# Kernel optimization log

Measured on AMD Instinct MI355X. Metric: run time of the kernel, lower is better.

Reference implementation:

```python
import jax, jax.numpy as jnp
import numpy as np

N = 50000
E = 640000
DIM_NODE = 128
DIM_HIDDEN = 128
DIM_FFN = 512
NUM_CLASSES = 10
NUM_GRAPHS = 128
NEG_SLOPE = 0.2


def setup_inputs() -> dict:
    key = jax.random.key(0)
    ks = jax.random.split(key, 24)
    g = lambda k, shape: jax.random.normal(k, shape, dtype=jnp.float32) * 0.05
    inp = {
        "x": jax.random.normal(ks[0], (N, DIM_NODE), dtype=jnp.float32),
        "edge_index": jax.random.randint(ks[1], (2, E), 0, N, dtype=jnp.int64),
        "batch": jnp.sort(jax.random.randint(ks[2], (N,), 0, NUM_GRAPHS, dtype=jnp.int64)),
        # GATConv 1: dim_node -> dim_hidden (heads=1)
        "W1": g(ks[3], (DIM_NODE, DIM_HIDDEN)),
        "as1": g(ks[4], (DIM_HIDDEN,)), "ad1": g(ks[5], (DIM_HIDDEN,)),
        "b1": g(ks[6], (DIM_HIDDEN,)),
        # GATConv 2
        "W2": g(ks[7], (DIM_HIDDEN, DIM_HIDDEN)),
        "as2": g(ks[8], (DIM_HIDDEN,)), "ad2": g(ks[9], (DIM_HIDDEN,)),
        "b2": g(ks[10], (DIM_HIDDEN,)),
        # GATConv 3
        "W3": g(ks[11], (DIM_HIDDEN, DIM_HIDDEN)),
        "as3": g(ks[12], (DIM_HIDDEN,)), "ad3": g(ks[13], (DIM_HIDDEN,)),
        "b3": g(ks[14], (DIM_HIDDEN,)),
        # FFN head
        "Wf1": g(ks[15], (DIM_HIDDEN, DIM_FFN)), "bf1": g(ks[16], (DIM_FFN,)),
        "Wf2": g(ks[17], (DIM_FFN, DIM_FFN)), "bf2": g(ks[18], (DIM_FFN,)),
        "Wf3": g(ks[19], (DIM_FFN, NUM_CLASSES)), "bf3": g(ks[20], (NUM_CLASSES,)),
    }
    return inp


def _gat_conv(x, src, dst, W, a_src, a_dst, bias):
    # x: [N, Fin]; src/dst: [E'] (self-loops included)
    h = x @ W                                  # [N, H]
    alpha_src = h @ a_src                      # [N]
    alpha_dst = h @ a_dst                      # [N]
    logits = jax.nn.leaky_relu(alpha_src[src] + alpha_dst[dst], NEG_SLOPE)  # [E']
    # segment softmax over incoming edges of each dst node
    m = jax.ops.segment_max(logits, dst, num_segments=N)
    ex = jnp.exp(logits - m[dst])
    denom = jax.ops.segment_sum(ex, dst, num_segments=N)
    alpha = ex / (denom[dst] + 1e-16)          # [E']
    out = jax.ops.segment_sum(alpha[:, None] * h[src], dst, num_segments=N)
    return out + bias


def reference(x, edge_index, batch, W1, as1, ad1, b1, W2, as2, ad2, b2,
              W3, as3, ad3, b3, Wf1, bf1, Wf2, bf2, Wf3, bf3):
    # PyG GATConv adds self-loops by default
    loops = jnp.arange(N, dtype=edge_index.dtype)
    src = jnp.concatenate([edge_index[0], loops])
    dst = jnp.concatenate([edge_index[1], loops])

    h = jax.nn.relu(_gat_conv(x, src, dst, W1, as1, ad1, b1))
    h = jax.nn.relu(_gat_conv(h, src, dst, W2, as2, ad2, b2))
    h = jax.nn.relu(_gat_conv(h, src, dst, W3, as3, ad3, b3))

    # global mean pool per graph
    sums = jax.ops.segment_sum(h, batch, num_segments=NUM_GRAPHS)
    cnts = jax.ops.segment_sum(jnp.ones((N,), h.dtype), batch, num_segments=NUM_GRAPHS)
    pooled = sums / jnp.maximum(cnts, 1.0)[:, None]   # [G, H]

    # FFN head (dropout is identity in eval)
    z = jax.nn.relu(pooled @ Wf1 + bf1)
    z = jax.nn.relu(z @ Wf2 + bf2)
    return z @ Wf3 + bf3                               # [G, num_classes]
```

## Files before the change

### kernel.cpp

```cpp
#include <hip/hip_runtime.h>

#define N_NODES 50000
#define N_EDGES 640000
#define TOT_E (N_EDGES + N_NODES)
#define NB 196
#define BCAP 4608
#define EPW 4096
#define NG 128
#define NCLS 10
#define NEG 0.2f

typedef unsigned int u32;
typedef unsigned short u16;
typedef __attribute__((ext_vector_type(8))) short s16x8;
typedef __attribute__((ext_vector_type(4))) float f32x4;

__device__ inline u32 bf16rne(float f) {
  u32 u = __float_as_uint(f);
  return (u + 0x7FFFu + ((u >> 16) & 1u)) >> 16;
}
__device__ inline float bf2f(u16 v) { return __uint_as_float((u32)v << 16); }

__global__ __launch_bounds__(256) void prep_kernel(int* __restrict__ bcur,
                                                   const float* __restrict__ W0,
                                                   const float* __restrict__ W1,
                                                   const float* __restrict__ W2,
                                                   u16* __restrict__ Wt) {
  int i = blockIdx.x * 256 + threadIdx.x;
  if (i < NB) bcur[i] = 0;
  if (i < 3 * 128 * 128) {
    int l = i >> 14, c = (i >> 7) & 127, k = i & 127;
    const float* W = (l == 0) ? W0 : ((l == 1) ? W1 : W2);
    Wt[i] = (u16)bf16rne(W[k * 128 + c]);
  }
}

__global__ __launch_bounds__(256) void scatter_kernel(const int* __restrict__ ei,
                                                      int* __restrict__ bcur,
                                                      u32* __restrict__ ebuf) {
  __shared__ int hist[NB], basee[NB], lcur[NB];
  int t = threadIdx.x;
  for (int b = t; b < NB; b += 256) hist[b] = 0;
  __syncthreads();
  int e0 = blockIdx.x * EPW;
  int e1 = min(TOT_E, e0 + EPW);
  for (int e = e0 + t; e < e1; e += 256) {
    int d = (e < N_EDGES) ? ei[N_EDGES + e] : (e - N_EDGES);
    atomicAdd(&hist[d >> 8], 1);
  }
  __syncthreads();
  for (int b = t; b < NB; b += 256) {
    int c = hist[b];
    basee[b] = (c > 0) ? atomicAdd(&bcur[b], c) : 0;
    lcur[b] = 0;
  }
  __syncthreads();
  for (int e = e0 + t; e < e1; e += 256) {
    int d, s;
    if (e < N_EDGES) { d = ei[N_EDGES + e]; s = ei[e]; }
    else { d = e - N_EDGES; s = d; }
    int b = d >> 8;
    int r = basee[b] + atomicAdd(&lcur[b], 1);
    if (r < BCAP) ebuf[(size_t)b * BCAP + r] = ((u32)d << 16) | (u32)s;
  }
}

__global__ __launch_bounds__(256) void degfill_kernel(const int* __restrict__ bcur,
                                                      const u32* __restrict__ ebuf,
                                                      u32* __restrict__ rldeg,
                                                      u16* __restrict__ col) {
  __shared__ int cnt[256], s[256], cur[256];
  int b = blockIdx.x, t = threadIdx.x;
  cnt[t] = 0; __syncthreads();
  int n = min(bcur[b], BCAP);
  const u32* eb = ebuf + (size_t)b * BCAP;
  for (int i = t; i < n; i += 256) atomicAdd(&cnt[(eb[i] >> 16) & 255], 1);
  __syncthreads();
  int v = cnt[t];
  s[t] = v; __syncthreads();
  for (int off = 1; off < 256; off <<= 1) {
    int tmp = (t >= off) ? s[t - off] : 0;
    __syncthreads();
    s[t] += tmp;
    __syncthreads();
  }
  int rl = s[t] - v;
  int node = (b << 8) + t;
  if (node < N_NODES) rldeg[node] = ((u32)rl << 16) | (u32)v;
  cur[t] = rl;
  __syncthreads();
  u16* cb = col + (size_t)b * BCAP;
  for (int i = t; i < n; i += 256) {
    u32 p = eb[i];
    int pos = atomicAdd(&cur[(p >> 16) & 255], 1);
    cb[pos] = (u16)(p & 0xFFFFu);
  }
}

template <bool CVT>
__global__ __launch_bounds__(64) void gemm_mfma(const void* __restrict__ Xin,
                                                const u16* __restrict__ Wt,
                                                const float* __restrict__ avs,
                                                const float* __restrict__ avd,
                                                u16* __restrict__ Hb,
                                                float* __restrict__ as_out,
                                                float* __restrict__ ad_out) {
  __shared__ u16 st[16 * 128];
  int lane = threadIdx.x;
  int m0 = blockIdx.x * 16;
  int ar = lane & 15, kg = lane >> 4;
  f32x4 acc[8];
#pragma unroll
  for (int n = 0; n < 8; n++) acc[n] = (f32x4){0.f, 0.f, 0.f, 0.f};
#pragma unroll
  for (int ks = 0; ks < 4; ks++) {
    s16x8 a;
    if (CVT) {
      const float* xr = (const float*)Xin + (size_t)(m0 + ar) * 128 + ks * 32 + kg * 8;
      float4 f0 = *(const float4*)xr;
      float4 f1 = *(const float4*)(xr + 4);
      a[0] = (short)bf16rne(f0.x); a[1] = (short)bf16rne(f0.y);
      a[2] = (short)bf16rne(f0.z); a[3] = (short)bf16rne(f0.w);
      a[4] = (short)bf16rne(f1.x); a[5] = (short)bf16rne(f1.y);
      a[6] = (short)bf16rne(f1.z); a[7] = (short)bf16rne(f1.w);
    } else {
      a = *(const s16x8*)((const u16*)Xin + (size_t)(m0 + ar) * 128 + ks * 32 + kg * 8);
    }
#pragma unroll
    for (int n = 0; n < 8; n++) {
      s16x8 b = *(const s16x8*)(Wt + (size_t)(n * 16 + ar) * 128 + ks * 32 + kg * 8);
      acc[n] = __builtin_amdgcn_mfma_f32_16x16x32_bf16(a, b, acc[n], 0, 0, 0);
    }
  }
  float avsv[8], advv[8];
#pragma unroll
  for (int n = 0; n < 8; n++) { avsv[n] = avs[n * 16 + ar]; advv[n] = avd[n * 16 + ar]; }
#pragma unroll
  for (int reg = 0; reg < 4; reg++) {
    float ps = 0.f, pd = 0.f;
#pragma unroll
    for (int n = 0; n < 8; n++) {
      ps = fmaf(acc[n][reg], avsv[n], ps);
      pd = fmaf(acc[n][reg], advv[n], pd);
    }
#pragma unroll
    for (int off = 1; off < 16; off <<= 1) {
      ps += __shfl_xor(ps, off, 64);
      pd += __shfl_xor(pd, off, 64);
    }
    if (ar == 0) {
      int row = m0 + kg * 4 + reg;
      as_out[row] = ps; ad_out[row] = pd;
    }
  }
#pragma unroll
  for (int n = 0; n < 8; n++)
#pragma unroll
    for (int reg = 0; reg < 4; reg++)
      st[(kg * 4 + reg) * 128 + n * 16 + ar] = (u16)bf16rne(acc[n][reg]);
  __syncthreads();
#pragma unroll
  for (int i = 0; i < 4; i++) {
    int u4 = i * 64 + lane;
    int r = u4 >> 4;
    int c8 = (u4 & 15) * 8;
    *(uint4*)(Hb + (size_t)(m0 + r) * 128 + c8) = *(const uint4*)&st[r * 128 + c8];
  }
}

__global__ __launch_bounds__(256) void agg_kernel(
    const u16* __restrict__ Hb, const float* __restrict__ asv,
    const float* __restrict__ adv, const u32* __restrict__ rldeg,
    const u16* __restrict__ col, const float* __restrict__ bias,
    u16* __restrict__ Ob) {
  int gid = blockIdx.x * blockDim.x + threadIdx.x;
  int node = gid >> 6;
  if (node >= N_NODES) return;
  int lane = threadIdx.x & 63;
  int q = lane >> 4;
  int li = lane & 15;
  u32 rd = rldeg[node];
  int r0 = (node >> 8) * BCAP + (int)(rd >> 16);
  int r1 = r0 + (int)(rd & 0xFFFFu);
  float ad = adv[node];
  float acc[8];
#pragma unroll
  for (int k = 0; k < 8; k++) acc[k] = 0.f;
  float den = 0.f;

  for (int base = r0; base < r1; base += 64) {
    int cnt = min(64, r1 - base);
    int s_l = 0; float ex_l = 0.f;
    if (lane < cnt) {
      s_l = (int)col[base + lane];
      float tt = asv[s_l] + ad;
      tt = (tt > 0.f) ? tt : NEG * tt;
      ex_l = __expf(tt);
    }
    float d = ex_l;
#pragma unroll
    for (int off = 32; off; off >>= 1) d += __shfl_xor(d, off, 64);
    den += d;

    int j = 0;
    for (; j + 8 <= cnt; j += 8) {
      int i0 = j + q, i1 = j + 4 + q;
      int s0 = __shfl(s_l, i0, 64); float e0 = __shfl(ex_l, i0, 64);
      int s1 = __shfl(s_l, i1, 64); float e1 = __shfl(ex_l, i1, 64);
      uint4 h0 = *(const uint4*)(Hb + (size_t)s0 * 128 + li * 8);
      uint4 h1 = *(const uint4*)(Hb + (size_t)s1 * 128 + li * 8);
      u32 w0[4] = {h0.x, h0.y, h0.z, h0.w};
      u32 w1[4] = {h1.x, h1.y, h1.z, h1.w};
#pragma unroll
      for (int k = 0; k < 4; k++) {
        acc[2 * k]     = fmaf(e0, __uint_as_float(w0[k] << 16), acc[2 * k]);
        acc[2 * k + 1] = fmaf(e0, __uint_as_float(w0[k] & 0xFFFF0000u), acc[2 * k + 1]);
      }
#pragma unroll
      for (int k = 0; k < 4; k++) {
        acc[2 * k]     = fmaf(e1, __uint_as_float(w1[k] << 16), acc[2 * k]);
        acc[2 * k + 1] = fmaf(e1, __uint_as_float(w1[k] & 0xFFFF0000u), acc[2 * k + 1]);
      }
    }
    for (; j < cnt; j += 4) {
      int i0 = j + q;
      int s0 = __shfl(s_l, i0, 64); float e0 = __shfl(ex_l, i0, 64);
      if (i0 < cnt) {
        uint4 h0 = *(const uint4*)(Hb + (size_t)s0 * 128 + li * 8);
        u32 w0[4] = {h0.x, h0.y, h0.z, h0.w};
#pragma unroll
        for (int k = 0; k < 4; k++) {
          acc[2 * k]     = fmaf(e0, __uint_as_float(w0[k] << 16), acc[2 * k]);
          acc[2 * k + 1] = fmaf(e0, __uint_as_float(w0[k] & 0xFFFF0000u), acc[2 * k + 1]);
        }
      }
    }
  }
#pragma unroll
  for (int k = 0; k < 8; k++) {
    acc[k] += __shfl_xor(acc[k], 16, 64);
    acc[k] += __shfl_xor(acc[k], 32, 64);
  }

  if (q == 0) {
    float inv = 1.f / (den + 1e-16f);
    float4 b0 = *(const float4*)(bias + li * 8);
    float4 b1 = *(const float4*)(bias + li * 8 + 4);
    float o[8];
    o[0] = fmaxf(fmaf(acc[0], inv, b0.x), 0.f);
    o[1] = fmaxf(fmaf(acc[1], inv, b0.y), 0.f);
    o[2] = fmaxf(fmaf(acc[2], inv, b0.z), 0.f);
    o[3] = fmaxf(fmaf(acc[3], inv, b0.w), 0.f);
    o[4] = fmaxf(fmaf(acc[4], inv, b1.x), 0.f);
    o[5] = fmaxf(fmaf(acc[5], inv, b1.y), 0.f);
    o[6] = fmaxf(fmaf(acc[6], inv, b1.z), 0.f);
    o[7] = fmaxf(fmaf(acc[7], inv, b1.w), 0.f);
    uint4 pb;
    pb.x = bf16rne(o[0]) | (bf16rne(o[1]) << 16);
    pb.y = bf16rne(o[2]) | (bf16rne(o[3]) << 16);
    pb.z = bf16rne(o[4]) | (bf16rne(o[5]) << 16);
    pb.w = bf16rne(o[6]) | (bf16rne(o[7]) << 16);
    *(uint4*)(Ob + (size_t)node * 128 + li * 8) = pb;
  }
}

__device__ inline int lbound(const int* b, int n, int v) {
  int lo = 0, hi = n;
  while (lo < hi) { int m = (lo + hi) >> 1; if (b[m] < v) lo = m + 1; else hi = m; }
  return lo;
}

__global__ __launch_bounds__(512) void ffn_fused(const u16* __restrict__ Ab,
                                                 const int* __restrict__ batch,
                                                 const float* __restrict__ Wf1,
                                                 const float* __restrict__ bf1,
                                                 const float* __restrict__ Wf2,
                                                 const float* __restrict__ bf2,
                                                 const float* __restrict__ Wf3,
                                                 const float* __restrict__ bf3,
                                                 float* __restrict__ out) {
  __shared__ float part[512];
  __shared__ float prow[128], z1s[512], z2s[512];
  int g = blockIdx.x, t = threadIdx.x;
  int lo = lbound(batch, N_NODES, g), hi = lbound(batch, N_NODES, g + 1);
  float cnt = fmaxf((float)(hi - lo), 1.f);
  int dim = t & 127, rg = t >> 7;
  float a = 0.f;
  for (int row = lo + rg; row < hi; row += 4)
    a += bf2f(Ab[(size_t)row * 128 + dim]);
  part[t] = a;
  __syncthreads();
  if (t < 128) prow[t] = (part[t] + part[t + 128] + part[t + 256] + part[t + 384]) / cnt;
  __syncthreads();
  float a1 = bf1[t];
  for (int k = 0; k < 128; ++k) a1 = fmaf(prow[k], Wf1[k * 512 + t], a1);
  z1s[t] = fmaxf(a1, 0.f);
  __syncthreads();
  float a2 = bf2[t];
  for (int k = 0; k < 512; ++k) a2 = fmaf(z1s[k], Wf2[k * 512 + t], a2);
  z2s[t] = fmaxf(a2, 0.f);
  __syncthreads();
  if (t < 160) {
    int c = t >> 4, l16 = t & 15;
    float p = 0.f;
#pragma unroll
    for (int j = 0; j < 32; ++j) {
      int k = l16 + 16 * j;
      p = fmaf(z2s[k], Wf3[k * NCLS + c], p);
    }
    p += __shfl_xor(p, 8, 16);
    p += __shfl_xor(p, 4, 16);
    p += __shfl_xor(p, 2, 16);
    p += __shfl_xor(p, 1, 16);
    if (l16 == 0) out[g * NCLS + c] = p + bf3[c];
  }
}

extern "C" void kernel_launch(void* const* d_in, const int* in_sizes, int n_in,
                              void* d_out, int out_size, void* d_ws, size_t ws_size,
                              hipStream_t stream) {
  const float* x   = (const float*)d_in[0];
  const int*   ei  = (const int*)d_in[1];
  const int*   bat = (const int*)d_in[2];
  const float* W[3]  = {(const float*)d_in[3], (const float*)d_in[7],  (const float*)d_in[11]};
  const float* As[3] = {(const float*)d_in[4], (const float*)d_in[8],  (const float*)d_in[12]};
  const float* Ad[3] = {(const float*)d_in[5], (const float*)d_in[9],  (const float*)d_in[13]};
  const float* B[3]  = {(const float*)d_in[6], (const float*)d_in[10], (const float*)d_in[14]};
  const float* Wf1 = (const float*)d_in[15]; const float* bf1 = (const float*)d_in[16];
  const float* Wf2 = (const float*)d_in[17]; const float* bf2 = (const float*)d_in[18];
  const float* Wf3 = (const float*)d_in[19]; const float* bf3 = (const float*)d_in[20];
  float* out = (float*)d_out;

  size_t off = 0;
  auto carve = [&](size_t bytes) {
    void* p = (char*)d_ws + off;
    off += (bytes + 255) & ~(size_t)255;
    return p;
  };
  u16*   Ab0    = (u16*)carve((size_t)N_NODES * 128 * 2);
  u16*   Ab1    = (u16*)carve((size_t)N_NODES * 128 * 2);
  u16*   Hb     = (u16*)carve((size_t)N_NODES * 128 * 2);
  u16*   Wt     = (u16*)carve((size_t)3 * 128 * 128 * 2);
  float* as_    = (float*)carve((size_t)N_NODES * 4);
  float* ad_    = (float*)carve((size_t)N_NODES * 4);
  u32*   rldeg  = (u32*)carve((size_t)N_NODES * 4);
  u16*   col    = (u16*)carve((size_t)NB * BCAP * 2);
  u32*   ebuf   = (u32*)carve((size_t)NB * BCAP * 4);
  int*   bcur   = (int*)carve(NB * 4);

  prep_kernel<<<192, 256, 0, stream>>>(bcur, W[0], W[1], W[2], Wt);

  int sgrid = (TOT_E + EPW - 1) / EPW;
  scatter_kernel<<<sgrid, 256, 0, stream>>>(ei, bcur, ebuf);
  degfill_kernel<<<NB, 256, 0, stream>>>(bcur, ebuf, rldeg, col);

  int node_waves_grid = (N_NODES * 64 + 255) / 256;
  gemm_mfma<true><<<3125, 64, 0, stream>>>(x, Wt, As[0], Ad[0], Hb, as_, ad_);
  agg_kernel<<<node_waves_grid, 256, 0, stream>>>(Hb, as_, ad_, rldeg, col, B[0], Ab0);
  gemm_mfma<false><<<3125, 64, 0, stream>>>(Ab0, Wt + 16384, As[1], Ad[1], Hb, as_, ad_);
  agg_kernel<<<node_waves_grid, 256, 0, stream>>>(Hb, as_, ad_, rldeg, col, B[1], Ab1);
  gemm_mfma<false><<<3125, 64, 0, stream>>>(Ab1, Wt + 32768, As[2], Ad[2], Hb, as_, ad_);
  agg_kernel<<<node_waves_grid, 256, 0, stream>>>(Hb, as_, ad_, rldeg, col, B[2], Ab0);

  ffn_fused<<<NG, 512, 0, stream>>>(Ab0, bat, Wf1, bf1, Wf2, bf2, Wf3, bf3, out);
}
```

Baseline: 238.7 us.

## Split pooling and FFN head into parallel multi-block kernels

```diff
diff --git a/kernel.cpp b/kernel.cpp
--- a/kernel.cpp
+++ b/kernel.cpp
@@ -9,6 +9,7 @@
 #define NG 128
 #define NCLS 10
 #define NEG 0.2f
+#define PCHUNK 50
 
 typedef unsigned int u32;
 typedef unsigned short u16;
@@ -22,16 +23,26 @@
 __device__ inline float bf2f(u16 v) { return __uint_as_float((u32)v << 16); }
 
 __global__ __launch_bounds__(256) void prep_kernel(int* __restrict__ bcur,
+                                                   float* __restrict__ psum,
+                                                   float* __restrict__ pcnt,
                                                    const float* __restrict__ W0,
                                                    const float* __restrict__ W1,
                                                    const float* __restrict__ W2,
-                                                   u16* __restrict__ Wt) {
+                                                   u16* __restrict__ Wt,
+                                                   const float* __restrict__ Wf3,
+                                                   float* __restrict__ Wf3t) {
   int i = blockIdx.x * 256 + threadIdx.x;
   if (i < NB) bcur[i] = 0;
+  if (i < NG * 128) psum[i] = 0.f;
+  if (i < NG) pcnt[i] = 0.f;
   if (i < 3 * 128 * 128) {
     int l = i >> 14, c = (i >> 7) & 127, k = i & 127;
     const float* W = (l == 0) ? W0 : ((l == 1) ? W1 : W2);
     Wt[i] = (u16)bf16rne(W[k * 128 + c]);
+  } else if (i < 3 * 128 * 128 + NCLS * 512) {
+    int j = i - 3 * 128 * 128;
+    int c = j >> 9, k = j & 511;
+    Wf3t[j] = Wf3[k * NCLS + c];
   }
 }
 
@@ -264,56 +275,90 @@
   }
 }
 
-__device__ inline int lbound(const int* b, int n, int v) {
-  int lo = 0, hi = n;
-  while (lo < hi) { int m = (lo + hi) >> 1; if (b[m] < v) lo = m + 1; else hi = m; }
-  return lo;
-}
-
-__global__ __launch_bounds__(512) void ffn_fused(const u16* __restrict__ Ab,
-                                                 const int* __restrict__ batch,
-                                                 const float* __restrict__ Wf1,
-                                                 const float* __restrict__ bf1,
-                                                 const float* __restrict__ Wf2,
-                                                 const float* __restrict__ bf2,
-                                                 const float* __restrict__ Wf3,
-                                                 const float* __restrict__ bf3,
-                                                 float* __restrict__ out) {
-  __shared__ float part[512];
-  __shared__ float prow[128], z1s[512], z2s[512];
-  int g = blockIdx.x, t = threadIdx.x;
-  int lo = lbound(batch, N_NODES, g), hi = lbound(batch, N_NODES, g + 1);
-  float cnt = fmaxf((float)(hi - lo), 1.f);
-  int dim = t & 127, rg = t >> 7;
+__global__ void pool_kernel(const u16* __restrict__ Hb, const int* __restrict__ batch,
+                            float* __restrict__ psum, float* __restrict__ pcnt) {
+  int t = threadIdx.x;
+  int start = blockIdx.x * PCHUNK;
+  int end = min(N_NODES, start + PCHUNK);
+  if (start >= end) return;
+  int cur = batch[start];
+  float acc = 0.f; int cnt = 0;
+  for (int i = start; i < end; ++i) {
+    int g = batch[i];
+    if (g != cur) {
+      atomicAdd(&psum[cur * 128 + t], acc);
+      if (t == 0) atomicAdd(&pcnt[cur], (float)cnt);
+      acc = 0.f; cnt = 0; cur = g;
+    }
+    acc += bf2f(Hb[(size_t)i * 128 + t]);
+    cnt++;
+  }
+  atomicAdd(&psum[cur * 128 + t], acc);
+  if (t == 0) atomicAdd(&pcnt[cur], (float)cnt);
+}
+
+__global__ __launch_bounds__(128) void ffn1_kernel(const float* __restrict__ psum,
+                                                   const float* __restrict__ pcnt,
+                                                   const float* __restrict__ Wf1,
+                                                   const float* __restrict__ bf1,
+                                                   float* __restrict__ z1) {
+  __shared__ float prow[128];
+  int b = blockIdx.x;
+  int g = b >> 2, ch = b & 3;
+  int t = threadIdx.x;
+  prow[t] = psum[g * 128 + t] / fmaxf(pcnt[g], 1.f);
+  __syncthreads();
+  int c = ch * 128 + t;
+  float a = bf1[c];
+#pragma unroll 8
+  for (int k = 0; k < 128; ++k) a = fmaf(prow[k], Wf1[k * 512 + c], a);
+  z1[g * 512 + c] = fmaxf(a, 0.f);
+}
+
+__global__ __launch_bounds__(256) void ffn2_kernel(const float* __restrict__ z1,
+                                                   const float* __restrict__ Wf2,
+                                                   const float* __restrict__ bf2,
+                                                   float* __restrict__ z2) {
+  __shared__ float z1s[512];
+  __shared__ float part[256];
+  int b = blockIdx.x;
+  int g = b >> 3, ch = b & 7;
+  int t = threadIdx.x;
+  z1s[t] = z1[g * 512 + t];
+  z1s[t + 256] = z1[g * 512 + t + 256];
+  __syncthreads();
+  int c = ch * 64 + (t & 63);
+  int kq = t >> 6;
   float a = 0.f;
-  for (int row = lo + rg; row < hi; row += 4)
-    a += bf2f(Ab[(size_t)row * 128 + dim]);
+#pragma unroll 8
+  for (int kk = 0; kk < 128; ++kk) {
+    int k = kq * 128 + kk;
+    a = fmaf(z1s[k], Wf2[k * 512 + c], a);
+  }
   part[t] = a;
   __syncthreads();
-  if (t < 128) prow[t] = (part[t] + part[t + 128] + part[t + 256] + part[t + 384]) / cnt;
-  __syncthreads();
-  float a1 = bf1[t];
-  for (int k = 0; k < 128; ++k) a1 = fmaf(prow[k], Wf1[k * 512 + t], a1);
-  z1s[t] = fmaxf(a1, 0.f);
-  __syncthreads();
-  float a2 = bf2[t];
-  for (int k = 0; k < 512; ++k) a2 = fmaf(z1s[k], Wf2[k * 512 + t], a2);
-  z2s[t] = fmaxf(a2, 0.f);
-  __syncthreads();
-  if (t < 160) {
-    int c = t >> 4, l16 = t & 15;
-    float p = 0.f;
-#pragma unroll
-    for (int j = 0; j < 32; ++j) {
-      int k = l16 + 16 * j;
-      p = fmaf(z2s[k], Wf3[k * NCLS + c], p);
-    }
-    p += __shfl_xor(p, 8, 16);
-    p += __shfl_xor(p, 4, 16);
-    p += __shfl_xor(p, 2, 16);
-    p += __shfl_xor(p, 1, 16);
-    if (l16 == 0) out[g * NCLS + c] = p + bf3[c];
-  }
+  if (kq == 0) {
+    float s = part[t] + part[t + 64] + part[t + 128] + part[t + 192] + bf2[c];
+    z2[g * 512 + c] = fmaxf(s, 0.f);
+  }
+}
+
+__global__ __launch_bounds__(256) void ffn3_kernel(const float* __restrict__ z2,
+                                                   const float* __restrict__ Wf3t,
+                                                   const float* __restrict__ bf3,
+                                                   float* __restrict__ out) {
+  int wid = blockIdx.x * 4 + (threadIdx.x >> 6);
+  int lane = threadIdx.x & 63;
+  int g = wid / NCLS, c = wid - g * NCLS;
+  float a = 0.f;
+#pragma unroll
+  for (int j = 0; j < 8; ++j) {
+    int k = j * 64 + lane;
+    a = fmaf(z2[g * 512 + k], Wf3t[c * 512 + k], a);
+  }
+#pragma unroll
+  for (int off = 32; off; off >>= 1) a += __shfl_xor(a, off, 64);
+  if (lane == 0) out[g * NCLS + c] = a + bf3[c];
 }
 
 extern "C" void kernel_launch(void* const* d_in, const int* in_sizes, int n_in,
@@ -347,8 +392,13 @@
   u16*   col    = (u16*)carve((size_t)NB * BCAP * 2);
   u32*   ebuf   = (u32*)carve((size_t)NB * BCAP * 4);
   int*   bcur   = (int*)carve(NB * 4);
-
-  prep_kernel<<<192, 256, 0, stream>>>(bcur, W[0], W[1], W[2], Wt);
+  float* psum   = (float*)carve(NG * 128 * 4);
+  float* pcnt   = (float*)carve(NG * 4);
+  float* z1     = (float*)carve(NG * 512 * 4);
+  float* z2     = (float*)carve(NG * 512 * 4);
+  float* Wf3t   = (float*)carve((size_t)NCLS * 512 * 4);
+
+  prep_kernel<<<256, 256, 0, stream>>>(bcur, psum, pcnt, W[0], W[1], W[2], Wt, Wf3, Wf3t);
 
   int sgrid = (TOT_E + EPW - 1) / EPW;
   scatter_kernel<<<sgrid, 256, 0, stream>>>(ei, bcur, ebuf);
@@ -362,5 +412,8 @@
   gemm_mfma<false><<<3125, 64, 0, stream>>>(Ab1, Wt + 32768, As[2], Ad[2], Hb, as_, ad_);
   agg_kernel<<<node_waves_grid, 256, 0, stream>>>(Hb, as_, ad_, rldeg, col, B[2], Ab0);
 
-  ffn_fused<<<NG, 512, 0, stream>>>(Ab0, bat, Wf1, bf1, Wf2, bf2, Wf3, bf3, out);
-}
+  pool_kernel<<<(N_NODES + PCHUNK - 1) / PCHUNK, 128, 0, stream>>>(Ab0, bat, psum, pcnt);
+  ffn1_kernel<<<NG * 4, 128, 0, stream>>>(psum, pcnt, Wf1, bf1, z1);
+  ffn2_kernel<<<NG * 8, 256, 0, stream>>>(z1, Wf2, bf2, z2);
+  ffn3_kernel<<<320, 256, 0, stream>>>(z2, Wf3t, bf3, out);
+}
```

Result: faster. 228.1 us (-4.5%).
